# Performance work log

Measured on AMD Instinct MI355X. Metric: run time of the kernel, lower is better.

## Reference

```python
import jax, jax.numpy as jnp
import numpy as np

N, M, E, F = 50000, 5000, 200000, 256  # nodes, hyperedges, incidences, channels


def setup_inputs() -> dict:
    key = jax.random.key(0)
    ks = jax.random.split(key, 7)
    x = jax.random.normal(ks[0], (N, F), dtype=jnp.float32)
    hyperedge_attr = jax.random.normal(ks[1], (M, F), dtype=jnp.float32)
    # glorot-ish scale for learned params
    weight = jax.random.normal(ks[2], (F, F), dtype=jnp.float32) * (1.0 / np.sqrt(F))
    att = jax.random.normal(ks[3], (2 * F,), dtype=jnp.float32) * 0.05
    bias = jnp.zeros((F,), dtype=jnp.float32)
    node_idx = jax.random.randint(ks[4], (E,), 0, N)  # hyperedge_index[0]
    edge_idx = jax.random.randint(ks[5], (E,), 0, M)  # hyperedge_index[1]
    return {"x": x, "hyperedge_attr": hyperedge_attr, "weight": weight,
            "att": att, "bias": bias, "node_idx": node_idx, "edge_idx": edge_idx}


def reference(x, hyperedge_attr, weight, att, bias, node_idx, edge_idx):
    # HypergraphConv.forward with use_attention=True, heads=1, concat=True,
    # hyperedge_weight=None (ones), EW_weight=None, dropout=0 (eval).
    n_nodes, feat = x.shape
    n_edges = hyperedge_attr.shape[0]

    he = hyperedge_attr @ weight                       # (M, F)

    # per-incidence attention score: (cat[x_i, he_j] * att).sum(-1)
    alpha = x[node_idx] @ att[:feat] + he[edge_idx] @ att[feat:]   # (E,)
    alpha = jax.nn.leaky_relu(alpha, 0.2)
    # segment softmax over source nodes (hyperedge_index[0])
    amax = jax.lax.stop_gradient(
        jax.ops.segment_max(alpha, node_idx, num_segments=n_nodes))
    ex = jnp.exp(alpha - amax[node_idx])
    denom = jax.ops.segment_sum(ex, node_idx, num_segments=n_nodes)
    alpha = ex / denom[node_idx]                       # (E,)

    ones_e = jnp.ones((node_idx.shape[0],), dtype=x.dtype)
    # D: node degree (hyperedge_weight==1); B: hyperedge cardinality
    D = jax.ops.segment_sum(ones_e, node_idx, num_segments=n_nodes)
    Dinv = jnp.where(D > 0, 1.0 / D, 0.0)
    B = jax.ops.segment_sum(ones_e, edge_idx, num_segments=n_edges)
    Binv = jnp.where(B > 0, 1.0 / B, 0.0)

    # propagate node -> hyperedge: msg = B_i * alpha * x_j, scatter_add at edge
    msg1 = (Binv[edge_idx] * alpha)[:, None] * x[node_idx]          # (E, F)
    edge_out = jax.ops.segment_sum(msg1, edge_idx, num_segments=n_edges)  # (M, F)

    # propagate hyperedge -> node: msg = D_i * alpha * e_j, scatter_add at node
    msg2 = (Dinv[node_idx] * alpha)[:, None] * edge_out[edge_idx]   # (E, F)
    node_out = jax.ops.segment_sum(msg2, node_idx, num_segments=n_nodes)  # (N, F)

    return jax.nn.leaky_relu(node_out + bias, 0.01)
```

## Files before the change

kernel.cpp:

```cpp
#include <hip/hip_runtime.h>
#include <math.h>

#define F 256
#define NODE_STRIDE 32
#define EDGE_STRIDE 128

typedef float f32x4 __attribute__((ext_vector_type(4)));
typedef unsigned short u16x8 __attribute__((ext_vector_type(8)));

__device__ __forceinline__ unsigned short f2bf(float f) {
    unsigned u = __float_as_uint(f);
    u = (u + 0x7FFFu + ((u >> 16) & 1u)) >> 16;
    return (unsigned short)u;
}
__device__ __forceinline__ float bf2f(unsigned short b) {
    return __uint_as_float((unsigned)b << 16);
}

__global__ void k_init_w2(const float* __restrict__ weight, const float* __restrict__ att,
                          float* __restrict__ w2,
                          float* denom, int* npos, int* epos, int N, int M) {
    int b = blockIdx.x, t = threadIdx.x;
    if (b < 64) {
        int wid = t >> 6, lane = t & 63;
        int row = b * 4 + wid;
        float4 wr = ((const float4*)(weight + (size_t)row * F))[lane];
        float4 av = ((const float4*)(att + F))[lane];
        float s = wr.x * av.x + wr.y * av.y + wr.z * av.z + wr.w * av.w;
        #pragma unroll
        for (int o = 32; o >= 1; o >>= 1) s += __shfl_down(s, o, 64);
        if (lane == 0) w2[row] = s;
    } else {
        int total = N > M ? N : M;
        int nth = (gridDim.x - 64) * blockDim.x;
        for (int i = (b - 64) * blockDim.x + t; i < total; i += nth) {
            if (i < N) { denom[i] = 0.0f; npos[i] = 0; }
            if (i < M) { epos[i] = 0; }
        }
    }
}

__global__ void k_rowdot(const float* __restrict__ x, const float* __restrict__ attr,
                         const float* __restrict__ att, const float* __restrict__ w2,
                         float* __restrict__ xa, float* __restrict__ hea,
                         unsigned short* __restrict__ xb,
                         int N, int M) {
    int wid  = (blockIdx.x * blockDim.x + threadIdx.x) >> 6;
    int lane = threadIdx.x & 63;
    if (wid >= N + M) return;
    const float* row;
    const float* vec;
    if (wid < N) { row = x    + (size_t)wid * F;       vec = att; }
    else         { row = attr + (size_t)(wid - N) * F; vec = w2;  }
    float4 rv = ((const float4*)row)[lane];
    float4 vv = ((const float4*)vec)[lane];
    if (wid < N) {
        ushort4 b4;
        b4.x = f2bf(rv.x); b4.y = f2bf(rv.y); b4.z = f2bf(rv.z); b4.w = f2bf(rv.w);
        ((ushort4*)(xb + (size_t)wid * F))[lane] = b4;
    }
    float s = rv.x * vv.x + rv.y * vv.y + rv.z * vv.z + rv.w * vv.w;
    #pragma unroll
    for (int o = 32; o >= 1; o >>= 1) s += __shfl_down(s, o, 64);
    if (lane == 0) {
        if (wid < N) xa[wid] = s;
        else         hea[wid - N] = s;
    }
}

__global__ void k_alpha_scatter(const float* __restrict__ xa, const float* __restrict__ hea,
                                const int* __restrict__ node_idx, const int* __restrict__ edge_idx,
                                float* denom, int* npos, int* epos,
                                int2* __restrict__ node_pairs, int2* __restrict__ edge_pairs,
                                int E) {
    int i = blockIdx.x * blockDim.x + threadIdx.x;
    int E4 = E >> 2;
    if (i < E4) {
        int4 nn = ((const int4*)node_idx)[i];
        int4 mm = ((const int4*)edge_idx)[i];
        float a0 = xa[nn.x] + hea[mm.x];
        float a1 = xa[nn.y] + hea[mm.y];
        float a2 = xa[nn.z] + hea[mm.z];
        float a3 = xa[nn.w] + hea[mm.w];
        a0 = a0 > 0.f ? a0 : 0.2f * a0;
        a1 = a1 > 0.f ? a1 : 0.2f * a1;
        a2 = a2 > 0.f ? a2 : 0.2f * a2;
        a3 = a3 > 0.f ? a3 : 0.2f * a3;
        float e0 = expf(a0), e1 = expf(a1), e2 = expf(a2), e3 = expf(a3);
        atomicAdd(&denom[nn.x], e0); atomicAdd(&denom[nn.y], e1);
        atomicAdd(&denom[nn.z], e2); atomicAdd(&denom[nn.w], e3);
        int p;
        p = atomicAdd(&npos[nn.x], 1); if (p < NODE_STRIDE) node_pairs[(size_t)nn.x * NODE_STRIDE + p] = make_int2(mm.x, __float_as_int(e0));
        p = atomicAdd(&npos[nn.y], 1); if (p < NODE_STRIDE) node_pairs[(size_t)nn.y * NODE_STRIDE + p] = make_int2(mm.y, __float_as_int(e1));
        p = atomicAdd(&npos[nn.z], 1); if (p < NODE_STRIDE) node_pairs[(size_t)nn.z * NODE_STRIDE + p] = make_int2(mm.z, __float_as_int(e2));
        p = atomicAdd(&npos[nn.w], 1); if (p < NODE_STRIDE) node_pairs[(size_t)nn.w * NODE_STRIDE + p] = make_int2(mm.w, __float_as_int(e3));
        p = atomicAdd(&epos[mm.x], 1); if (p < EDGE_STRIDE) edge_pairs[(size_t)mm.x * EDGE_STRIDE + p] = make_int2(nn.x, __float_as_int(e0));
        p = atomicAdd(&epos[mm.y], 1); if (p < EDGE_STRIDE) edge_pairs[(size_t)mm.y * EDGE_STRIDE + p] = make_int2(nn.y, __float_as_int(e1));
        p = atomicAdd(&epos[mm.z], 1); if (p < EDGE_STRIDE) edge_pairs[(size_t)mm.z * EDGE_STRIDE + p] = make_int2(nn.z, __float_as_int(e2));
        p = atomicAdd(&epos[mm.w], 1); if (p < EDGE_STRIDE) edge_pairs[(size_t)mm.w * EDGE_STRIDE + p] = make_int2(nn.w, __float_as_int(e3));
    } else if (i == E4) {
        for (int e = E4 * 4; e < E; ++e) {
            int n = node_idx[e], m = edge_idx[e];
            float a = xa[n] + hea[m];
            a = a > 0.f ? a : 0.2f * a;
            float ex = expf(a);
            atomicAdd(&denom[n], ex);
            int p = atomicAdd(&npos[n], 1);
            if (p < NODE_STRIDE) node_pairs[(size_t)n * NODE_STRIDE + p] = make_int2(m, __float_as_int(ex));
            int q = atomicAdd(&epos[m], 1);
            if (q < EDGE_STRIDE) edge_pairs[(size_t)m * EDGE_STRIDE + q] = make_int2(n, __float_as_int(ex));
        }
    }
}

__global__ void k_edge_gather(const unsigned short* __restrict__ xb,
                              const float* __restrict__ denom,
                              const int2* __restrict__ edge_pairs,
                              const int* __restrict__ epos,
                              unsigned short* __restrict__ edge_out, int M) {
    int wid = threadIdx.x >> 6, lane = threadIdx.x & 63;
    int half = lane >> 5, fl = lane & 31;
    __shared__ float part[3][32][8];
    for (int m = blockIdx.x; m < M; m += gridDim.x) {
        int B = epos[m];
        int cnt = B < EDGE_STRIDE ? B : EDGE_STRIDE;
        const int2* pairs = edge_pairs + (size_t)m * EDGE_STRIDE;
        float acc[8] = {0.f, 0.f, 0.f, 0.f, 0.f, 0.f, 0.f, 0.f};
        for (int base = wid * 16; base < cnt; base += 64) {
            int li = base + (lane & 15);
            int2 pl = pairs[li < cnt ? li : cnt - 1];
            float wl = __int_as_float(pl.y) / denom[pl.x];
            int rem = cnt - base; if (rem > 16) rem = 16;
            #pragma unroll
            for (int k = 0; k < 8; ++k) {
                int pi = 2 * k + half;
                if (pi < rem) {
                    int   nj = __shfl(pl.x, pi, 16);
                    float wj = __shfl(wl,   pi, 16);
                    u16x8 v = ((const u16x8*)(xb + (size_t)nj * F))[fl];
                    #pragma unroll
                    for (int q = 0; q < 8; ++q) acc[q] += wj * bf2f(v[q]);
                }
            }
        }
        #pragma unroll
        for (int q = 0; q < 8; ++q) acc[q] += __shfl_xor(acc[q], 32, 64);
        if (wid > 0 && half == 0) {
            #pragma unroll
            for (int q = 0; q < 8; ++q) part[wid - 1][fl][q] = acc[q];
        }
        __syncthreads();
        if (wid == 0 && half == 0) {
            #pragma unroll
            for (int w = 0; w < 3; ++w)
                #pragma unroll
                for (int q = 0; q < 8; ++q) acc[q] += part[w][fl][q];
            float Binv = (B > 0) ? 1.0f / (float)B : 0.0f;
            u16x8 r;
            #pragma unroll
            for (int q = 0; q < 8; ++q) r[q] = f2bf(acc[q] * Binv);
            ((u16x8*)(edge_out + (size_t)m * F))[fl] = r;
        }
        __syncthreads();
    }
}

__global__ void k_node_gather(const unsigned short* __restrict__ edge_out,
                              const int2* __restrict__ node_pairs,
                              const float* __restrict__ bias,
                              const int* __restrict__ npos,
                              const float* __restrict__ denom,
                              float* __restrict__ out, int N) {
    int wid = threadIdx.x >> 6, lane = threadIdx.x & 63;
    int half = lane >> 5, fl = lane & 31;
    f32x4 b0 = ((const f32x4*)bias)[fl * 2];
    f32x4 b1 = ((const f32x4*)bias)[fl * 2 + 1];
    for (int n = blockIdx.x * 4 + wid; n < N; n += gridDim.x * 4) {
        int D = npos[n];
        int cnt = D < NODE_STRIDE ? D : NODE_STRIDE;
        const int2* pairs = node_pairs + (size_t)n * NODE_STRIDE;
        float acc[8] = {0.f, 0.f, 0.f, 0.f, 0.f, 0.f, 0.f, 0.f};
        for (int base = 0; base < cnt; base += 16) {
            int li = base + (lane & 15);
            int2 pl = pairs[li < cnt ? li : cnt - 1];
            float wl = __int_as_float(pl.y);
            int rem = cnt - base; if (rem > 16) rem = 16;
            #pragma unroll
            for (int k = 0; k < 8; ++k) {
                int pi = 2 * k + half;
                if (pi < rem) {
                    int   mj = __shfl(pl.x, pi, 16);
                    float wj = __shfl(wl,   pi, 16);
                    u16x8 v = ((const u16x8*)(edge_out + (size_t)mj * F))[fl];
                    #pragma unroll
                    for (int q = 0; q < 8; ++q) acc[q] += wj * bf2f(v[q]);
                }
            }
        }
        #pragma unroll
        for (int q = 0; q < 8; ++q) acc[q] += __shfl_xor(acc[q], 32, 64);
        if (half == 0) {
            float scale = (D > 0) ? 1.0f / ((float)D * denom[n]) : 0.0f;
            f32x4 r0, r1;
            r0.x = acc[0] * scale + b0.x; r0.y = acc[1] * scale + b0.y;
            r0.z = acc[2] * scale + b0.z; r0.w = acc[3] * scale + b0.w;
            r1.x = acc[4] * scale + b1.x; r1.y = acc[5] * scale + b1.y;
            r1.z = acc[6] * scale + b1.z; r1.w = acc[7] * scale + b1.w;
            r0.x = r0.x > 0.f ? r0.x : 0.01f * r0.x;
            r0.y = r0.y > 0.f ? r0.y : 0.01f * r0.y;
            r0.z = r0.z > 0.f ? r0.z : 0.01f * r0.z;
            r0.w = r0.w > 0.f ? r0.w : 0.01f * r0.w;
            r1.x = r1.x > 0.f ? r1.x : 0.01f * r1.x;
            r1.y = r1.y > 0.f ? r1.y : 0.01f * r1.y;
            r1.z = r1.z > 0.f ? r1.z : 0.01f * r1.z;
            r1.w = r1.w > 0.f ? r1.w : 0.01f * r1.w;
            __builtin_nontemporal_store(r0, (f32x4*)(out + (size_t)n * F) + fl * 2);
            __builtin_nontemporal_store(r1, (f32x4*)(out + (size_t)n * F) + fl * 2 + 1);
        }
    }
}

extern "C" void kernel_launch(void* const* d_in, const int* in_sizes, int n_in,
                              void* d_out, int out_size, void* d_ws, size_t ws_size,
                              hipStream_t stream) {
    const float* x        = (const float*)d_in[0];
    const float* attr     = (const float*)d_in[1];
    const float* weight   = (const float*)d_in[2];
    const float* att      = (const float*)d_in[3];
    const float* bias     = (const float*)d_in[4];
    const int*   node_idx = (const int*)d_in[5];
    const int*   edge_idx = (const int*)d_in[6];

    const int Fdim = in_sizes[4];
    const int N = in_sizes[0] / Fdim;
    const int M = in_sizes[1] / Fdim;
    const int E = in_sizes[5];
    float* out = (float*)d_out;

    char* ws = (char*)d_ws;
    auto alloc = [&](size_t bytes) -> void* {
        void* p = (void*)ws;
        ws += ((bytes + 255) / 256) * 256;
        return p;
    };
    float*          w2         = (float*)alloc((size_t)Fdim * 4);
    float*          xa         = (float*)alloc((size_t)N * 4);
    float*          hea        = (float*)alloc((size_t)M * 4);
    float*          denom      = (float*)alloc((size_t)N * 4);
    int*            npos       = (int*)alloc((size_t)N * 4);
    int*            epos       = (int*)alloc((size_t)M * 4);
    unsigned short* xb         = (unsigned short*)alloc((size_t)N * Fdim * 2);
    int2*           node_pairs = (int2*)alloc((size_t)N * NODE_STRIDE * 8);
    int2*           edge_pairs = (int2*)alloc((size_t)M * EDGE_STRIDE * 8);
    unsigned short* edge_out   = (unsigned short*)alloc((size_t)M * Fdim * 2);

    hipLaunchKernelGGL(k_init_w2, dim3(256), dim3(256), 0, stream,
                       weight, att, w2, denom, npos, epos, N, M);
    int rows = N + M;
    hipLaunchKernelGGL(k_rowdot, dim3((rows + 3) / 4), dim3(256), 0, stream,
                       x, attr, att, w2, xa, hea, xb, N, M);
    int E4 = E / 4;
    hipLaunchKernelGGL(k_alpha_scatter, dim3((E4 + 1 + 255) / 256), dim3(256), 0, stream,
                       xa, hea, node_idx, edge_idx, denom, npos, epos,
                       node_pairs, edge_pairs, E);
    int egrid = M < 2048 ? M : 2048;
    hipLaunchKernelGGL(k_edge_gather, dim3(egrid), dim3(256), 0, stream,
                       xb, denom, edge_pairs, epos, edge_out, M);
    int ngrid = 2048;
    hipLaunchKernelGGL(k_node_gather, dim3(ngrid), dim3(256), 0, stream,
                       edge_out, node_pairs, bias, npos, denom, out, N);
}
```

Before: 97.60 us.

## Remap gathers: one wave per hyperedge, one half-wave per node

The edge gather now gives each hyperedge to a single wave instead of a whole block. Each half-wave takes alternating 16-pair chunks, which removes the shared-memory partial reduction and both block barriers. The node gather now gives each node to one half-wave that walks all of its pairs. This removes the cross-half shuffle reduction and lets both halves store results. The aim is to cut sync overhead and idle lanes at low average degree (about 40 pairs per edge, about 4 per node), at the cost of less parallelism within a node and more serial loop trips per lane.

```diff
diff --git a/kernel.cpp b/kernel.cpp
--- a/kernel.cpp
+++ b/kernel.cpp
@@ -120,23 +120,22 @@
                               unsigned short* __restrict__ edge_out, int M) {
     int wid = threadIdx.x >> 6, lane = threadIdx.x & 63;
     int half = lane >> 5, fl = lane & 31;
-    __shared__ float part[3][32][8];
-    for (int m = blockIdx.x; m < M; m += gridDim.x) {
+    int nwaves = gridDim.x * 4;
+    for (int m = blockIdx.x * 4 + wid; m < M; m += nwaves) {
         int B = epos[m];
         int cnt = B < EDGE_STRIDE ? B : EDGE_STRIDE;
         const int2* pairs = edge_pairs + (size_t)m * EDGE_STRIDE;
         float acc[8] = {0.f, 0.f, 0.f, 0.f, 0.f, 0.f, 0.f, 0.f};
-        for (int base = wid * 16; base < cnt; base += 64) {
-            int li = base + (lane & 15);
+        for (int base = half * 16; base < cnt; base += 32) {
+            int li = base + (fl & 15);
             int2 pl = pairs[li < cnt ? li : cnt - 1];
             float wl = __int_as_float(pl.y) / denom[pl.x];
             int rem = cnt - base; if (rem > 16) rem = 16;
             #pragma unroll
-            for (int k = 0; k < 8; ++k) {
-                int pi = 2 * k + half;
-                if (pi < rem) {
-                    int   nj = __shfl(pl.x, pi, 16);
-                    float wj = __shfl(wl,   pi, 16);
+            for (int j = 0; j < 16; ++j) {
+                if (j < rem) {
+                    int   nj = __shfl(pl.x, j, 32);
+                    float wj = __shfl(wl,   j, 32);
                     u16x8 v = ((const u16x8*)(xb + (size_t)nj * F))[fl];
                     #pragma unroll
                     for (int q = 0; q < 8; ++q) acc[q] += wj * bf2f(v[q]);
@@ -145,23 +144,13 @@
         }
         #pragma unroll
         for (int q = 0; q < 8; ++q) acc[q] += __shfl_xor(acc[q], 32, 64);
-        if (wid > 0 && half == 0) {
-            #pragma unroll
-            for (int q = 0; q < 8; ++q) part[wid - 1][fl][q] = acc[q];
-        }
-        __syncthreads();
-        if (wid == 0 && half == 0) {
-            #pragma unroll
-            for (int w = 0; w < 3; ++w)
-                #pragma unroll
-                for (int q = 0; q < 8; ++q) acc[q] += part[w][fl][q];
+        if (half == 0) {
             float Binv = (B > 0) ? 1.0f / (float)B : 0.0f;
             u16x8 r;
             #pragma unroll
             for (int q = 0; q < 8; ++q) r[q] = f2bf(acc[q] * Binv);
             ((u16x8*)(edge_out + (size_t)m * F))[fl] = r;
         }
-        __syncthreads();
     }
 }
 
@@ -175,48 +164,44 @@
     int half = lane >> 5, fl = lane & 31;
     f32x4 b0 = ((const f32x4*)bias)[fl * 2];
     f32x4 b1 = ((const f32x4*)bias)[fl * 2 + 1];
-    for (int n = blockIdx.x * 4 + wid; n < N; n += gridDim.x * 4) {
+    int nhalves = gridDim.x * 8;
+    for (int n = blockIdx.x * 8 + wid * 2 + half; n < N; n += nhalves) {
         int D = npos[n];
         int cnt = D < NODE_STRIDE ? D : NODE_STRIDE;
         const int2* pairs = node_pairs + (size_t)n * NODE_STRIDE;
         float acc[8] = {0.f, 0.f, 0.f, 0.f, 0.f, 0.f, 0.f, 0.f};
         for (int base = 0; base < cnt; base += 16) {
-            int li = base + (lane & 15);
+            int li = base + (fl & 15);
             int2 pl = pairs[li < cnt ? li : cnt - 1];
             float wl = __int_as_float(pl.y);
             int rem = cnt - base; if (rem > 16) rem = 16;
             #pragma unroll
-            for (int k = 0; k < 8; ++k) {
-                int pi = 2 * k + half;
-                if (pi < rem) {
-                    int   mj = __shfl(pl.x, pi, 16);
-                    float wj = __shfl(wl,   pi, 16);
+            for (int j = 0; j < 16; ++j) {
+                if (j < rem) {
+                    int   mj = __shfl(pl.x, j, 32);
+                    float wj = __shfl(wl,   j, 32);
                     u16x8 v = ((const u16x8*)(edge_out + (size_t)mj * F))[fl];
                     #pragma unroll
                     for (int q = 0; q < 8; ++q) acc[q] += wj * bf2f(v[q]);
                 }
             }
         }
-        #pragma unroll
-        for (int q = 0; q < 8; ++q) acc[q] += __shfl_xor(acc[q], 32, 64);
-        if (half == 0) {
-            float scale = (D > 0) ? 1.0f / ((float)D * denom[n]) : 0.0f;
-            f32x4 r0, r1;
-            r0.x = acc[0] * scale + b0.x; r0.y = acc[1] * scale + b0.y;
-            r0.z = acc[2] * scale + b0.z; r0.w = acc[3] * scale + b0.w;
-            r1.x = acc[4] * scale + b1.x; r1.y = acc[5] * scale + b1.y;
-            r1.z = acc[6] * scale + b1.z; r1.w = acc[7] * scale + b1.w;
-            r0.x = r0.x > 0.f ? r0.x : 0.01f * r0.x;
-            r0.y = r0.y > 0.f ? r0.y : 0.01f * r0.y;
-            r0.z = r0.z > 0.f ? r0.z : 0.01f * r0.z;
-            r0.w = r0.w > 0.f ? r0.w : 0.01f * r0.w;
-            r1.x = r1.x > 0.f ? r1.x : 0.01f * r1.x;
-            r1.y = r1.y > 0.f ? r1.y : 0.01f * r1.y;
-            r1.z = r1.z > 0.f ? r1.z : 0.01f * r1.z;
-            r1.w = r1.w > 0.f ? r1.w : 0.01f * r1.w;
-            __builtin_nontemporal_store(r0, (f32x4*)(out + (size_t)n * F) + fl * 2);
-            __builtin_nontemporal_store(r1, (f32x4*)(out + (size_t)n * F) + fl * 2 + 1);
-        }
+        float scale = (D > 0) ? 1.0f / ((float)D * denom[n]) : 0.0f;
+        f32x4 r0, r1;
+        r0.x = acc[0] * scale + b0.x; r0.y = acc[1] * scale + b0.y;
+        r0.z = acc[2] * scale + b0.z; r0.w = acc[3] * scale + b0.w;
+        r1.x = acc[4] * scale + b1.x; r1.y = acc[5] * scale + b1.y;
+        r1.z = acc[6] * scale + b1.z; r1.w = acc[7] * scale + b1.w;
+        r0.x = r0.x > 0.f ? r0.x : 0.01f * r0.x;
+        r0.y = r0.y > 0.f ? r0.y : 0.01f * r0.y;
+        r0.z = r0.z > 0.f ? r0.z : 0.01f * r0.z;
+        r0.w = r0.w > 0.f ? r0.w : 0.01f * r0.w;
+        r1.x = r1.x > 0.f ? r1.x : 0.01f * r1.x;
+        r1.y = r1.y > 0.f ? r1.y : 0.01f * r1.y;
+        r1.z = r1.z > 0.f ? r1.z : 0.01f * r1.z;
+        r1.w = r1.w > 0.f ? r1.w : 0.01f * r1.w;
+        __builtin_nontemporal_store(r0, (f32x4*)(out + (size_t)n * F) + fl * 2);
+        __builtin_nontemporal_store(r1, (f32x4*)(out + (size_t)n * F) + fl * 2 + 1);
     }
 }
 
@@ -263,10 +248,9 @@
     hipLaunchKernelGGL(k_alpha_scatter, dim3((E4 + 1 + 255) / 256), dim3(256), 0, stream,
                        xa, hea, node_idx, edge_idx, denom, npos, epos,
                        node_pairs, edge_pairs, E);
-    int egrid = M < 2048 ? M : 2048;
+    int egrid = (M + 3) / 4;
     hipLaunchKernelGGL(k_edge_gather, dim3(egrid), dim3(256), 0, stream,
                        xb, denom, edge_pairs, epos, edge_out, M);
-    int ngrid = 2048;
-    hipLaunchKernelGGL(k_node_gather, dim3(ngrid), dim3(256), 0, stream,
+    hipLaunchKernelGGL(k_node_gather, dim3(2048), dim3(256), 0, stream,
                        edge_out, node_pairs, bias, npos, denom, out, N);
 }
```

Measured after the change: 97.47 us. Within noise of the previous version (-0.1%).
